# Kernel optimization log

Measured on AMD Instinct MI355X. Metric: run time of the kernel, lower is better.

## Reference

```python
import jax, jax.numpy as jnp
import numpy as np

B, L, D, K = 64, 1024, 128, 256
SQRT_2D = float(np.sqrt(2 * D))


def _biamlp(x1, x2, Wi, bi, Wq, bq):
    # proj to 2*D, norm-weighted fusion, avg-pool(2)*2 (== pairwise sum), L2-normalize over dim 1
    f1 = x1 @ Wi + bi          # [B, L, 2D]
    f2 = x2 @ Wq + bq          # [B, L, 2D]
    n1 = jnp.linalg.norm(f1)   # global L2 norm (scalar), as torch.norm(., p=2)
    n2 = jnp.linalg.norm(f2)
    e = (n1 / (n1 + n2)) * f1 + (n2 / (n1 + n2)) * f2
    b, l, c = e.shape
    z = e.reshape(b, l, c // 2, 2).mean(-1) * 2.0   # AvgPool1d(2,2) * 2 -> [B, L, D]
    denom = jnp.maximum(jnp.linalg.norm(z, axis=1, keepdims=True), 1e-12)  # F.normalize dim=1
    return z / denom


def _branch(feats, G_src, W_aff, W_c, W_lin, W_h):
    # feats: [B, L, D]; G_src: [B, L, 2D] (tensor fed to the affine projection)
    # a_j = affine(G_src^T): [B, 2D, L] @ [L, L]
    a_j = jnp.einsum('blc,lm->bcm', G_src, W_aff)            # [B, 2D, L]
    att = jnp.einsum('bld,bcl->bdc', feats, a_j) / SQRT_2D    # [B, D, 2D]
    C = jnp.tanh(att)
    H = jax.nn.relu(C @ W_c + jnp.einsum('bld,lk->bdk', feats, W_lin))  # [B, D, K]
    out = jnp.swapaxes(H @ W_h, 1, 2) + feats                 # [B, L, D]
    return out


def setup_inputs() -> dict:
    key = jax.random.key(0)
    ks = jax.random.split(key, 22)
    s = 0.02
    inp = {
        'f1_norm': jax.random.normal(ks[0], (B, L, D), jnp.float32),
        'f2_norm': jax.random.normal(ks[1], (B, L, D), jnp.float32),
        'f3_norm': jax.random.normal(ks[2], (B, L, D), jnp.float32),
        # BiAMLP params (feat_size = 128)
        'Wi': jax.random.normal(ks[3], (D, 2 * D), jnp.float32) * s,
        'bi': jax.random.normal(ks[4], (2 * D,), jnp.float32) * s,
        'Wq': jax.random.normal(ks[5], (D, 2 * D), jnp.float32) * s,
        'bq': jax.random.normal(ks[6], (2 * D,), jnp.float32) * s,
        # affine_{a,v,l}: Linear(l, l, bias=False), stored [in, out]
        'Wa_aff': jax.random.normal(ks[7], (L, L), jnp.float32) * s,
        'Wv_aff': jax.random.normal(ks[8], (L, L), jnp.float32) * s,
        'Wl_aff': jax.random.normal(ks[9], (L, L), jnp.float32) * s,
        # W_{a,v,t}: Linear(l, k)
        'W_a': jax.random.normal(ks[10], (L, K), jnp.float32) * s,
        'W_v': jax.random.normal(ks[11], (L, K), jnp.float32) * s,
        'W_t': jax.random.normal(ks[12], (L, K), jnp.float32) * s,
        # W_c{a,v,t}: Linear(2d, k)
        'W_ca': jax.random.normal(ks[13], (2 * D, K), jnp.float32) * s,
        'W_cv': jax.random.normal(ks[14], (2 * D, K), jnp.float32) * s,
        'W_ct': jax.random.normal(ks[15], (2 * D, K), jnp.float32) * s,
        # W_h{a,v,t}: Linear(k, l)
        'W_ha': jax.random.normal(ks[16], (K, L), jnp.float32) * s,
        'W_hv': jax.random.normal(ks[17], (K, L), jnp.float32) * s,
        'W_ht': jax.random.normal(ks[18], (K, L), jnp.float32) * s,
    }
    return inp


def reference(f1_norm, f2_norm, f3_norm, Wi, bi, Wq, bq, Wa_aff, Wv_aff, Wl_aff,
              W_a, W_v, W_t, W_ca, W_cv, W_ct, W_ha, W_hv, W_ht):
    txt, aud, vis = f1_norm, f2_norm, f3_norm
    # G2 = mode(txt, vis) and G3 = mode(aud, vis) are computed but unused in the
    # original (dead code); only G = G1 affects the output.
    G = _biamlp(txt, aud, Wi, bi, Wq, bq)        # [B, L, D]
    G_ag = jnp.concatenate([aud, G], axis=2)     # [B, L, 2D]
    G_lg = jnp.concatenate([txt, G], axis=2)     # [B, L, 2D]
    # NOTE: original bug preserved -- the visual branch projects G_ag (not G_vg).
    aud_out = _branch(aud, G_ag, Wa_aff, W_ca, W_a, W_ha)
    vis_out = _branch(vis, G_ag, Wv_aff, W_cv, W_v, W_hv)
    txt_out = _branch(txt, G_lg, Wl_aff, W_ct, W_t, W_ht)
    return (txt_out, aud_out, vis_out)
```

## Files before the change

### kernel.cpp

```cpp
#include <hip/hip_runtime.h>
#include <math.h>

typedef __attribute__((ext_vector_type(8))) short bf16x8;
typedef __attribute__((ext_vector_type(4))) float f32x4;

static constexpr int B_ = 64, L_ = 1024, D_ = 128, K_ = 256;
static constexpr long BLD_ = (long)B_ * L_ * D_;
static constexpr long LD_  = (long)L_ * D_;

__device__ __forceinline__ unsigned short f2b(float f) {
    unsigned int u = __builtin_bit_cast(unsigned int, f);
    u = (u + 0x7fffu + ((u >> 16) & 1u)) >> 16;
    return (unsigned short)u;
}
__device__ __forceinline__ float b2f(unsigned short h) {
    unsigned int u = ((unsigned int)h) << 16;
    return __builtin_bit_cast(float, u);
}

__device__ __forceinline__ void gl16(const unsigned short* g, unsigned short* s) {
    __builtin_amdgcn_global_load_lds(
        (const __attribute__((address_space(1))) unsigned int*)g,
        (__attribute__((address_space(3))) unsigned int*)s, 16, 0, 0);
}

struct TrEnt { const float* src; unsigned short* dst; int R, C, nb, start; };
struct TrTab { TrEnt e[14]; };

__global__ __launch_bounds__(256)
void trk(TrTab tab)
{
    __shared__ unsigned short T[64][72];
    int bid = blockIdx.x;
    int ei = 0;
    #pragma unroll
    for (int i = 1; i < 14; ++i) if (bid >= tab.e[i].start) ei = i;
    TrEnt e = tab.e[ei];
    int tile = bid - e.start;
    int ntR = e.R >> 6, ntC = e.C >> 6;
    int nt = ntR * ntC;
    int bb = tile / nt, tt = tile - bb * nt;
    int ri = tt % ntR, ci = tt / ntR;
    const float* src = e.src + (long)bb * e.R * e.C + (long)(ri * 64) * e.C + ci * 64;
    unsigned short* dst = e.dst + (long)bb * e.R * e.C + (long)(ci * 64) * e.R + ri * 64;
    int t = threadIdx.x;
    {
        int r = t >> 2, cq = t & 3;
        const float* s = src + (long)r * e.C + cq * 16;
        unsigned short tmp[16];
        #pragma unroll
        for (int f = 0; f < 4; ++f) {
            float4 v = *(const float4*)(s + f * 4);
            tmp[f*4+0]=f2b(v.x); tmp[f*4+1]=f2b(v.y); tmp[f*4+2]=f2b(v.z); tmp[f*4+3]=f2b(v.w);
        }
        *(uint4*)&T[r][cq*16]   = *(uint4*)&tmp[0];
        *(uint4*)&T[r][cq*16+8] = *(uint4*)&tmp[8];
    }
    __syncthreads();
    {
        int cr = t >> 2, rq = t & 3;
        unsigned short tmp[16];
        #pragma unroll
        for (int j = 0; j < 16; ++j) tmp[j] = T[rq*16 + j][cr];
        unsigned short* dp = dst + (long)cr * e.R + rq * 16;
        *(uint4*)&dp[0] = *(uint4*)&tmp[0];
        *(uint4*)&dp[8] = *(uint4*)&tmp[8];
    }
}

__global__ __launch_bounds__(256)
void cvt3(const float* s0, const float* s1, const float* s2,
          unsigned short* d, long n)
{
    const float* s = blockIdx.y == 0 ? s0 : blockIdx.y == 1 ? s1 : s2;
    unsigned short* dd = d + (long)blockIdx.y * n;
    long i = ((long)blockIdx.x * 256 + threadIdx.x) * 4;
    long stride = (long)gridDim.x * 1024;
    for (; i < n; i += stride) {
        float4 v = *(const float4*)&s[i];
        unsigned int w0 = (unsigned int)f2b(v.x) | ((unsigned int)f2b(v.y) << 16);
        unsigned int w1 = (unsigned int)f2b(v.z) | ((unsigned int)f2b(v.w) << 16);
        uint2 w; w.x = w0; w.y = w1;
        *(uint2*)&dd[i] = w;
    }
}

struct OpDesc {
    const unsigned short* A;
    long aOff0, aOff1, aOff2, sA;
    int lda;
    const unsigned short* B0;
    long bOff0, bOff1, bOff2, sB0;
    const unsigned short* B1;
    long sB1;
    int ldb;
    void* C;
    long sC;
    int ldc;
    const float* E0; const float* E1; const float* E2;
    float* ss;
    int Kd;
};

template<int EPI, int AF32, int TM>
__device__ __forceinline__ void gbody(const OpDesc& d, int bx, int by, int zrem,
                                      unsigned short (*As)[TM][32],
                                      unsigned short (*Bs)[128][32])
{
    const int tid = threadIdx.x;
    const long m0 = (long)bx * TM;
    const int n0 = by * 128;
    const int br = zrem >> 6, bb = zrem & 63;

    long aO = (br == 0 ? d.aOff0 : br == 1 ? d.aOff1 : d.aOff2) + (long)bb * d.sA;
    const unsigned short* A_ = d.A + aO;
    const float* Af = (const float*)d.A;
    const unsigned short* Bp;
    int nB = n0;
    if (d.B1 && n0 >= 128) { Bp = d.B1 + (long)bb * d.sB1; nB = n0 - 128; }
    else { Bp = d.B0 + (br == 0 ? d.bOff0 : br == 1 ? d.bOff1 : d.bOff2) + (long)bb * d.sB0; }

    const int w = tid >> 6, l = tid & 63;
    const int wm = (TM == 128) ? (w >> 1) : 0;
    const int wn = (TM == 128) ? (w & 1) : w;
    const int NJ = (TM == 128) ? 4 : 2;
    const int WS = (TM == 128) ? 64 : 32;
    const int fr = l & 15, kg = l >> 4;

    f32x4 acc[4][4];
    #pragma unroll
    for (int i = 0; i < 4; ++i)
        #pragma unroll
        for (int j = 0; j < 4; ++j)
            acc[i][j] = (f32x4){0.f, 0.f, 0.f, 0.f};

    auto stage = [&](int buf, int k0) {
        if (AF32) {
            int row = tid >> 1, half = tid & 1;
            const float* s = Af + (long)(m0 + row) * d.lda + k0 + half * 16;
            unsigned short tmp[16];
            #pragma unroll
            for (int f = 0; f < 4; ++f) {
                float4 v = *(const float4*)(s + f * 4);
                tmp[f*4+0]=f2b(v.x); tmp[f*4+1]=f2b(v.y); tmp[f*4+2]=f2b(v.z); tmp[f*4+3]=f2b(v.w);
            }
            *(uint4*)&As[buf][row][half*16]     = *(uint4*)&tmp[0];
            *(uint4*)&As[buf][row][half*16 + 8] = *(uint4*)&tmp[8];
        } else if (TM == 128) {
            const unsigned short* ga = A_ + (m0 + 32*w + (l >> 2)) * (long)d.lda + k0 + (l & 3) * 8;
            gl16(ga,                    &As[buf][32*w][0]);
            gl16(ga + 16*(long)d.lda,   &As[buf][32*w + 16][0]);
        } else {
            const unsigned short* ga = A_ + (m0 + 16*w + (l >> 2)) * (long)d.lda + k0 + (l & 3) * 8;
            gl16(ga, &As[buf][16*w][0]);
        }
        const unsigned short* gb = Bp + (long)(nB + 32*w + (l >> 2)) * d.ldb + k0 + (l & 3) * 8;
        gl16(gb,                  &Bs[buf][32*w][0]);
        gl16(gb + 16*(long)d.ldb, &Bs[buf][32*w + 16][0]);
    };

    auto compute = [&](int cb) {
        bf16x8 af[4], bf[4];
        #pragma unroll
        for (int i = 0; i < 4; ++i) af[i] = *(const bf16x8*)&As[cb][wm*64 + i*16 + fr][kg*8];
        #pragma unroll
        for (int j = 0; j < NJ; ++j) bf[j] = *(const bf16x8*)&Bs[cb][wn*WS + j*16 + fr][kg*8];
        #pragma unroll
        for (int i = 0; i < 4; ++i)
            #pragma unroll
            for (int j = 0; j < NJ; ++j)
                acc[i][j] = __builtin_amdgcn_mfma_f32_16x16x32_bf16(af[i], bf[j], acc[i][j], 0, 0, 0);
    };

    const int nt = d.Kd >> 5;
    stage(0, 0);
    __syncthreads();
    for (int t = 0; t < nt; ++t) {
        if (t + 1 < nt) stage((t + 1) & 1, (t + 1) << 5);
        compute(t & 1);
        __syncthreads();
    }

    if (EPI == 4) {
        unsigned short* C = (unsigned short*)d.C;
        float lss = 0.f;
        #pragma unroll
        for (int i = 0; i < 4; ++i) {
            #pragma unroll
            for (int j = 0; j < 4; ++j) {
                int cg = n0 + wn*64 + j*16 + fr;
                float bias = d.E0[cg];
                #pragma unroll
                for (int r = 0; r < 4; ++r) {
                    float v = acc[i][j][r] + bias;
                    lss += v * v;
                    float vp = v + __shfl_xor(v, 1);
                    if (!(fr & 1)) {
                        long row = m0 + wm*64 + i*16 + kg*4 + r;
                        C[row * (long)d.ldc + (cg >> 1)] = f2b(vp);
                    }
                }
            }
        }
        #pragma unroll
        for (int o = 32; o; o >>= 1) lss += __shfl_xor(lss, o);
        __shared__ float red4[4];
        if (l == 0) red4[w] = lss;
        __syncthreads();
        if (tid == 0)
            d.ss[bx * 2 + by] = red4[0] + red4[1] + red4[2] + red4[3];
    } else if (TM == 64) {
        float* eb = (float*)As;
        #pragma unroll
        for (int cc = 0; cc < 4; ++cc) {
            __syncthreads();
            #pragma unroll
            for (int j = 0; j < 2; ++j)
                #pragma unroll
                for (int r = 0; r < 4; ++r)
                    eb[(kg*4 + r)*128 + wn*32 + j*16 + fr] = acc[cc][j][r];
            __syncthreads();
            unsigned short* C = (unsigned short*)d.C + (long)zrem * d.sC;
            int colx = (tid & 15) * 8;
            int lr = tid >> 4;
            long gr = m0 + cc*16 + lr;
            long gi = gr * (long)d.ldc + n0 + colx;
            unsigned short ov[8];
            if (EPI == 2) *(uint4*)ov = *(const uint4*)&C[gi];
            unsigned short pk[8];
            #pragma unroll
            for (int e = 0; e < 8; ++e) {
                float v = eb[lr*128 + colx + e];
                if (EPI == 1) v = tanhf(v * 0.0625f);
                if (EPI == 2) v = fmaxf(v + b2f(ov[e]), 0.f);
                pk[e] = f2b(v);
            }
            *(uint4*)&C[gi] = *(uint4*)&pk[0];
        }
    } else {
        float* eb = (float*)As;
        #pragma unroll
        for (int cc = 0; cc < 4; ++cc) {
            __syncthreads();
            #pragma unroll
            for (int j = 0; j < 4; ++j)
                #pragma unroll
                for (int r = 0; r < 4; ++r)
                    eb[(wm*16 + kg*4 + r)*128 + wn*64 + j*16 + fr] = acc[cc][j][r];
            __syncthreads();
            if (EPI == 3) {
                long off = (br == 2) ? 0L : (long)(br + 1) * BLD_;
                float* Co = (float*)d.C + off + (long)bb * LD_;
                const float* Ep = (br == 0 ? d.E0 : br == 1 ? d.E1 : d.E2) + (long)bb * LD_;
                int colx = (tid & 31) * 4;
                #pragma unroll
                for (int p = 0; p < 4; ++p) {
                    int lr = (tid >> 5) + 8 * p;
                    long gr = m0 + (lr < 16 ? cc*16 + lr : 48 + cc*16 + lr);
                    long gi = gr * (long)d.ldc + n0 + colx;
                    float4 v = *(float4*)&eb[lr*128 + colx];
                    float4 e4 = *(const float4*)&Ep[gi];
                    v.x += e4.x; v.y += e4.y; v.z += e4.z; v.w += e4.w;
                    *(float4*)&Co[gi] = v;
                }
            } else {
                unsigned short* C = (unsigned short*)d.C + (long)zrem * d.sC;
                int colx = (tid & 15) * 8;
                #pragma unroll
                for (int p = 0; p < 2; ++p) {
                    int lr = (tid >> 4) + 16 * p;
                    long gr = m0 + (lr < 16 ? cc*16 + lr : 48 + cc*16 + lr);
                    long gi = gr * (long)d.ldc + n0 + colx;
                    unsigned short ov[8];
                    if (EPI == 2) *(uint4*)ov = *(const uint4*)&C[gi];
                    unsigned short pk[8];
                    #pragma unroll
                    for (int e = 0; e < 8; ++e) {
                        float v = eb[lr*128 + colx + e];
                        if (EPI == 1) v = tanhf(v * 0.0625f);
                        if (EPI == 2) v = fmaxf(v + b2f(ov[e]), 0.f);
                        pk[e] = f2b(v);
                    }
                    *(uint4*)&C[gi] = *(uint4*)&pk[0];
                }
            }
        }
    }
}

template<int EPI0, int EPI1, int AF32, int SWZ, int TM>
__global__ __launch_bounds__(256)
void mg(OpDesc d0, OpDesc d1, int zsplit)
{
    __shared__ __align__(16) unsigned short As[2][TM][32];
    __shared__ __align__(16) unsigned short Bs[2][128][32];
    int bx, by, bz;
    if (SWZ) {
        int nwg = gridDim.x * gridDim.y * gridDim.z;
        int c = blockIdx.x + gridDim.x * (blockIdx.y + gridDim.y * blockIdx.z);
        int lid = (c & 7) * (nwg >> 3) + (c >> 3);
        bx = lid % gridDim.x; lid /= gridDim.x;
        by = lid % gridDim.y; bz = lid / gridDim.y;
    } else {
        bx = blockIdx.x; by = blockIdx.y; bz = blockIdx.z;
    }
    if (bz < zsplit) gbody<EPI0, AF32, TM>(d0, bx, by, bz, As, Bs);
    else             gbody<EPI1, AF32, TM>(d1, bx, by, bz - zsplit, As, Bs);
}

__global__ __launch_bounds__(256)
void k2z(unsigned short* __restrict__ q1, const unsigned short* __restrict__ q2,
         const float* __restrict__ partial, float* __restrict__ colssP)
{
    int t = threadIdx.x;
    float a = partial[t] + partial[t + 256] + partial[t + 512] + partial[t + 768];
    float bsum = partial[1024 + t] + partial[1280 + t] + partial[1536 + t] + partial[1792 + t];
    #pragma unroll
    for (int o = 32; o; o >>= 1) { a += __shfl_xor(a, o); bsum += __shfl_xor(bsum, o); }
    __shared__ float ra[4], rb[4];
    int wv = t >> 6;
    if ((t & 63) == 0) { ra[wv] = a; rb[wv] = bsum; }
    __syncthreads();
    float n1 = sqrtf(ra[0] + ra[1] + ra[2] + ra[3]);
    float n2 = sqrtf(rb[0] + rb[1] + rb[2] + rb[3]);
    float al = n1 / (n1 + n2), be = n2 / (n1 + n2);

    int b = blockIdx.x, lc = blockIdx.y;
    int d = t & 127, ls = t >> 7;
    long base = ((long)b * L_ + (long)lc * 64) * D_;
    float acc = 0.f;
    for (int ll = ls; ll < 64; ll += 2) {
        long idx = base + (long)ll * D_ + d;
        float zv = al * b2f(q1[idx]) + be * b2f(q2[idx]);
        q1[idx] = f2b(zv);
        acc += zv * zv;
    }
    __shared__ float red[256];
    red[t] = acc;
    __syncthreads();
    if (t < 128)
        colssP[((long)b * 16 + lc) * 128 + d] = red[t] + red[t + 128];
}

__global__ __launch_bounds__(256)
void k3nT(const unsigned short* __restrict__ z, const float* __restrict__ colssP,
          unsigned short* __restrict__ GT)
{
    __shared__ unsigned short T[128][136];
    int b = blockIdx.x, lt = blockIdx.y;
    int t = threadIdx.x;
    {
        int r = t >> 1, half = t & 1;
        const unsigned short* src = z + ((long)b * L_ + lt * 128 + r) * D_ + half * 64;
        #pragma unroll
        for (int q = 0; q < 8; ++q)
            *(uint4*)&T[r][half*64 + q*8] = *(const uint4*)(src + q*8);
    }
    __syncthreads();
    {
        int d = t >> 1, lh = t & 1;
        float s = 0.f;
        #pragma unroll
        for (int lc = 0; lc < 16; ++lc)
            s += colssP[((long)b * 16 + lc) * 128 + d];
        float inv = 1.f / fmaxf(sqrtf(s), 1e-12f);
        unsigned short tmp[64];
        #pragma unroll
        for (int j = 0; j < 64; ++j) tmp[j] = f2b(b2f(T[lh*64 + j][d]) * inv);
        unsigned short* dp = GT + ((long)b * D_ + d) * L_ + lt * 128 + lh * 64;
        #pragma unroll
        for (int q = 0; q < 8; ++q) *(uint4*)&dp[q*8] = *(uint4*)&tmp[q*8];
    }
}

extern "C" void kernel_launch(void* const* d_in, const int* in_sizes, int n_in,
                              void* d_out, int out_size, void* d_ws, size_t ws_size,
                              hipStream_t stream)
{
    const float* txt = (const float*)d_in[0];
    const float* aud = (const float*)d_in[1];
    const float* vis = (const float*)d_in[2];
    const float* Wi  = (const float*)d_in[3];
    const float* bi  = (const float*)d_in[4];
    const float* Wq  = (const float*)d_in[5];
    const float* bq  = (const float*)d_in[6];
    const float* Waff[3] = { (const float*)d_in[7], (const float*)d_in[8], (const float*)d_in[9] };
    const float* Wlin[3] = { (const float*)d_in[10], (const float*)d_in[11], (const float*)d_in[12] };
    const float* Wc[3]   = { (const float*)d_in[13], (const float*)d_in[14], (const float*)d_in[15] };
    const float* Wh[3]   = { (const float*)d_in[16], (const float*)d_in[17], (const float*)d_in[18] };

    unsigned short* w16 = (unsigned short*)d_ws;
    unsigned short* featT = w16;
    unsigned short* q1b   = featT + 3 * BLD_;
    unsigned short* q2b   = q1b + BLD_;
    unsigned short* WAb   = q2b + BLD_;
    unsigned short* WLTb  = WAb + 3145728;
    unsigned short* WCTb  = WLTb + 786432;
    unsigned short* WHTb  = WCTb + 196608;
    unsigned short* WiTb  = WHTb + 786432;
    unsigned short* WqTb  = WiTb + 32768;
    float* partial = (float*)(WqTb + 32768);
    float* colssP  = partial + 2048;
    unsigned short* Cm3 = q1b;
    unsigned short* Hb3 = q1b + 6291456;
    unsigned short* S2all = (unsigned short*)d_out;
    unsigned short* GT    = S2all + 3 * BLD_;

    TrTab tab;
    auto setE = [&](int i, const float* s, unsigned short* dst, int R, int C, int nb, int start) {
        tab.e[i].src = s; tab.e[i].dst = dst; tab.e[i].R = R; tab.e[i].C = C;
        tab.e[i].nb = nb; tab.e[i].start = start;
    };
    int st = 0;
    setE(0, aud, featT + 0,        1024, 128, 64, st); st += 2048;
    setE(1, vis, featT + BLD_,     1024, 128, 64, st); st += 2048;
    setE(2, txt, featT + 2 * BLD_, 1024, 128, 64, st); st += 2048;
    setE(3, Wi, WiTb, 128, 256, 1, st); st += 8;
    setE(4, Wq, WqTb, 128, 256, 1, st); st += 8;
    for (int i = 0; i < 3; ++i) { setE(5 + i, Wlin[i], WLTb + (long)i * 262144, 1024, 256, 1, st); st += 64; }
    for (int i = 0; i < 3; ++i) { setE(8 + i, Wc[i],   WCTb + (long)i * 65536,  256, 256, 1, st); st += 16; }
    for (int i = 0; i < 3; ++i) { setE(11 + i, Wh[i],  WHTb + (long)i * 262144, 256, 1024, 1, st); st += 64; }
    trk<<<st, 256, 0, stream>>>(tab);
    cvt3<<<dim3(1024, 3), 256, 0, stream>>>(Waff[0], Waff[1], Waff[2], WAb, 1048576);

    OpDesc dTxt = {}, dAud = {};
    dTxt.A = (const unsigned short*)txt; dTxt.lda = 128;
    dTxt.B0 = WiTb; dTxt.ldb = 128;
    dTxt.C = q1b; dTxt.ldc = 128;
    dTxt.E0 = bi; dTxt.ss = partial; dTxt.Kd = 128;
    dAud = dTxt;
    dAud.A = (const unsigned short*)aud; dAud.B0 = WqTb; dAud.C = q2b;
    dAud.E0 = bq; dAud.ss = partial + 1024;
    mg<4, 4, 1, 0, 128><<<dim3(512, 2, 2), 256, 0, stream>>>(dTxt, dAud, 1);

    k2z<<<dim3(64, 16), 256, 0, stream>>>(q1b, q2b, partial, colssP);
    k3nT<<<dim3(64, 8), 256, 0, stream>>>(q1b, colssP, GT);

    OpDesc dS2 = {};
    dS2.A = featT; dS2.aOff0 = 0; dS2.aOff1 = BLD_; dS2.aOff2 = 2 * BLD_;
    dS2.sA = LD_; dS2.lda = 1024;
    dS2.B0 = WAb; dS2.bOff0 = 0; dS2.bOff1 = 1048576; dS2.bOff2 = 2097152;
    dS2.sB0 = 0; dS2.ldb = 1024;
    dS2.C = S2all; dS2.sC = LD_; dS2.ldc = 1024; dS2.Kd = 1024;
    mg<0, 0, 0, 1, 128><<<dim3(1, 8, 192), 256, 0, stream>>>(dS2, dS2, 192);

    OpDesc dAtt = {};
    dAtt.A = S2all; dAtt.aOff0 = 0; dAtt.aOff1 = 64 * LD_; dAtt.aOff2 = 128 * LD_;
    dAtt.sA = LD_; dAtt.lda = 1024;
    dAtt.B0 = featT; dAtt.bOff0 = 0; dAtt.bOff1 = 0; dAtt.bOff2 = 2 * BLD_;
    dAtt.sB0 = LD_;
    dAtt.B1 = GT; dAtt.sB1 = LD_; dAtt.ldb = 1024;
    dAtt.C = Cm3; dAtt.sC = 32768; dAtt.ldc = 256; dAtt.Kd = 1024;
    OpDesc dU = {};
    dU.A = featT; dU.aOff0 = 0; dU.aOff1 = BLD_; dU.aOff2 = 2 * BLD_;
    dU.sA = LD_; dU.lda = 1024;
    dU.B0 = WLTb; dU.bOff0 = 0; dU.bOff1 = 262144; dU.bOff2 = 524288;
    dU.sB0 = 0; dU.ldb = 1024;
    dU.C = Hb3; dU.sC = 32768; dU.ldc = 256; dU.Kd = 1024;
    mg<1, 0, 0, 1, 64><<<dim3(2, 2, 384), 256, 0, stream>>>(dAtt, dU, 192);

    OpDesc dT = {};
    dT.A = Cm3; dT.aOff0 = 0; dT.aOff1 = 2097152; dT.aOff2 = 4194304;
    dT.sA = 32768; dT.lda = 256;
    dT.B0 = WCTb; dT.bOff0 = 0; dT.bOff1 = 65536; dT.bOff2 = 131072;
    dT.sB0 = 0; dT.ldb = 256;
    dT.C = Hb3; dT.sC = 32768; dT.ldc = 256; dT.Kd = 256;
    mg<2, 2, 0, 1, 64><<<dim3(2, 2, 192), 256, 0, stream>>>(dT, dT, 192);

    OpDesc dOut = {};
    dOut.A = WHTb; dOut.aOff0 = 0; dOut.aOff1 = 262144; dOut.aOff2 = 524288;
    dOut.sA = 0; dOut.lda = 256;
    dOut.B0 = Hb3; dOut.bOff0 = 0; dOut.bOff1 = 2097152; dOut.bOff2 = 4194304;
    dOut.sB0 = 32768; dOut.ldb = 256;
    dOut.C = d_out; dOut.ldc = 128;
    dOut.E0 = aud; dOut.E1 = vis; dOut.E2 = txt; dOut.Kd = 256;
    mg<3, 3, 0, 1, 128><<<dim3(8, 1, 192), 256, 0, stream>>>(dOut, dOut, 192);
}
```

Baseline: 294.7 us.

## Swizzle LDS tiles, stage EPI4 output through LDS, fold weight convert into transpose kernel

The GEMM kernel now XOR-swizzles the column chunk index in both the global-to-LDS loads and the fragment reads, to reduce LDS bank conflicts. The EPI==4 projection epilogue writes biased accumulators to LDS and then emits packed 16-byte rows of pairwise sums, replacing the scattered 2-byte stores that used shuffles. The separate cvt3 launch for the affine weights is removed and those weights go through the transpose kernel as non-transposed entries, saving one launch. The LDS staging adds extra barriers in the epilogue, and the swizzle must agree exactly between the load and read paths.

After: 296.7 us. No clear change (+0.7%).

```diff
diff --git a/kernel.cpp b/kernel.cpp
--- a/kernel.cpp
+++ b/kernel.cpp
@@ -24,8 +24,8 @@
         (__attribute__((address_space(3))) unsigned int*)s, 16, 0, 0);
 }
 
-struct TrEnt { const float* src; unsigned short* dst; int R, C, nb, start; };
-struct TrTab { TrEnt e[14]; };
+struct TrEnt { const float* src; unsigned short* dst; int R, C, tr, start; };
+struct TrTab { TrEnt e[17]; };
 
 __global__ __launch_bounds__(256)
 void trk(TrTab tab)
@@ -34,7 +34,7 @@
     int bid = blockIdx.x;
     int ei = 0;
     #pragma unroll
-    for (int i = 1; i < 14; ++i) if (bid >= tab.e[i].start) ei = i;
+    for (int i = 1; i < 17; ++i) if (bid >= tab.e[i].start) ei = i;
     TrEnt e = tab.e[ei];
     int tile = bid - e.start;
     int ntR = e.R >> 6, ntC = e.C >> 6;
@@ -42,8 +42,23 @@
     int bb = tile / nt, tt = tile - bb * nt;
     int ri = tt % ntR, ci = tt / ntR;
     const float* src = e.src + (long)bb * e.R * e.C + (long)(ri * 64) * e.C + ci * 64;
+    int t = threadIdx.x;
+    if (!e.tr) {
+        unsigned short* dstd = e.dst + (long)bb * e.R * e.C + (long)(ri * 64) * e.C + ci * 64;
+        int r = t >> 2, cq = t & 3;
+        const float* s = src + (long)r * e.C + cq * 16;
+        unsigned short tmp[16];
+        #pragma unroll
+        for (int f = 0; f < 4; ++f) {
+            float4 v = *(const float4*)(s + f * 4);
+            tmp[f*4+0]=f2b(v.x); tmp[f*4+1]=f2b(v.y); tmp[f*4+2]=f2b(v.z); tmp[f*4+3]=f2b(v.w);
+        }
+        unsigned short* dp = dstd + (long)r * e.C + cq * 16;
+        *(uint4*)&dp[0] = *(uint4*)&tmp[0];
+        *(uint4*)&dp[8] = *(uint4*)&tmp[8];
+        return;
+    }
     unsigned short* dst = e.dst + (long)bb * e.R * e.C + (long)(ci * 64) * e.R + ri * 64;
-    int t = threadIdx.x;
     {
         int r = t >> 2, cq = t & 3;
         const float* s = src + (long)r * e.C + cq * 16;
@@ -65,23 +80,6 @@
         unsigned short* dp = dst + (long)cr * e.R + rq * 16;
         *(uint4*)&dp[0] = *(uint4*)&tmp[0];
         *(uint4*)&dp[8] = *(uint4*)&tmp[8];
-    }
-}
-
-__global__ __launch_bounds__(256)
-void cvt3(const float* s0, const float* s1, const float* s2,
-          unsigned short* d, long n)
-{
-    const float* s = blockIdx.y == 0 ? s0 : blockIdx.y == 1 ? s1 : s2;
-    unsigned short* dd = d + (long)blockIdx.y * n;
-    long i = ((long)blockIdx.x * 256 + threadIdx.x) * 4;
-    long stride = (long)gridDim.x * 1024;
-    for (; i < n; i += stride) {
-        float4 v = *(const float4*)&s[i];
-        unsigned int w0 = (unsigned int)f2b(v.x) | ((unsigned int)f2b(v.y) << 16);
-        unsigned int w1 = (unsigned int)f2b(v.z) | ((unsigned int)f2b(v.w) << 16);
-        uint2 w; w.x = w0; w.y = w1;
-        *(uint2*)&dd[i] = w;
     }
 }
 
@@ -134,6 +132,9 @@
         for (int j = 0; j < 4; ++j)
             acc[i][j] = (f32x4){0.f, 0.f, 0.f, 0.f};
 
+    const int sc8 = ((l & 3) ^ ((l >> 3) & 3)) * 8;
+    const int rc  = (kg ^ ((fr >> 1) & 3)) * 8;
+
     auto stage = [&](int buf, int k0) {
         if (AF32) {
             int row = tid >> 1, half = tid & 1;
@@ -144,17 +145,18 @@
                 float4 v = *(const float4*)(s + f * 4);
                 tmp[f*4+0]=f2b(v.x); tmp[f*4+1]=f2b(v.y); tmp[f*4+2]=f2b(v.z); tmp[f*4+3]=f2b(v.w);
             }
-            *(uint4*)&As[buf][row][half*16]     = *(uint4*)&tmp[0];
-            *(uint4*)&As[buf][row][half*16 + 8] = *(uint4*)&tmp[8];
+            int sw = (row >> 1) & 3;
+            *(uint4*)&As[buf][row][((2*half    ) ^ sw) * 8] = *(uint4*)&tmp[0];
+            *(uint4*)&As[buf][row][((2*half + 1) ^ sw) * 8] = *(uint4*)&tmp[8];
         } else if (TM == 128) {
-            const unsigned short* ga = A_ + (m0 + 32*w + (l >> 2)) * (long)d.lda + k0 + (l & 3) * 8;
+            const unsigned short* ga = A_ + (m0 + 32*w + (l >> 2)) * (long)d.lda + k0 + sc8;
             gl16(ga,                    &As[buf][32*w][0]);
             gl16(ga + 16*(long)d.lda,   &As[buf][32*w + 16][0]);
         } else {
-            const unsigned short* ga = A_ + (m0 + 16*w + (l >> 2)) * (long)d.lda + k0 + (l & 3) * 8;
+            const unsigned short* ga = A_ + (m0 + 16*w + (l >> 2)) * (long)d.lda + k0 + sc8;
             gl16(ga, &As[buf][16*w][0]);
         }
-        const unsigned short* gb = Bp + (long)(nB + 32*w + (l >> 2)) * d.ldb + k0 + (l & 3) * 8;
+        const unsigned short* gb = Bp + (long)(nB + 32*w + (l >> 2)) * d.ldb + k0 + sc8;
         gl16(gb,                  &Bs[buf][32*w][0]);
         gl16(gb + 16*(long)d.ldb, &Bs[buf][32*w + 16][0]);
     };
@@ -162,9 +164,9 @@
     auto compute = [&](int cb) {
         bf16x8 af[4], bf[4];
         #pragma unroll
-        for (int i = 0; i < 4; ++i) af[i] = *(const bf16x8*)&As[cb][wm*64 + i*16 + fr][kg*8];
-        #pragma unroll
-        for (int j = 0; j < NJ; ++j) bf[j] = *(const bf16x8*)&Bs[cb][wn*WS + j*16 + fr][kg*8];
+        for (int i = 0; i < 4; ++i) af[i] = *(const bf16x8*)&As[cb][wm*64 + i*16 + fr][rc];
+        #pragma unroll
+        for (int j = 0; j < NJ; ++j) bf[j] = *(const bf16x8*)&Bs[cb][wn*WS + j*16 + fr][rc];
         #pragma unroll
         for (int i = 0; i < 4; ++i)
             #pragma unroll
@@ -185,7 +187,7 @@
         unsigned short* C = (unsigned short*)d.C;
         float lss = 0.f;
         #pragma unroll
-        for (int i = 0; i < 4; ++i) {
+        for (int i = 0; i < 4; ++i)
             #pragma unroll
             for (int j = 0; j < 4; ++j) {
                 int cg = n0 + wn*64 + j*16 + fr;
@@ -194,19 +196,36 @@
                 for (int r = 0; r < 4; ++r) {
                     float v = acc[i][j][r] + bias;
                     lss += v * v;
-                    float vp = v + __shfl_xor(v, 1);
-                    if (!(fr & 1)) {
-                        long row = m0 + wm*64 + i*16 + kg*4 + r;
-                        C[row * (long)d.ldc + (cg >> 1)] = f2b(vp);
-                    }
                 }
             }
-        }
         #pragma unroll
         for (int o = 32; o; o >>= 1) lss += __shfl_xor(lss, o);
         __shared__ float red4[4];
         if (l == 0) red4[w] = lss;
-        __syncthreads();
+        float* eb = (float*)As;
+        #pragma unroll
+        for (int cc = 0; cc < 4; ++cc) {
+            __syncthreads();
+            #pragma unroll
+            for (int j = 0; j < 4; ++j) {
+                int cg = n0 + wn*64 + j*16 + fr;
+                float bias = d.E0[cg];
+                #pragma unroll
+                for (int r = 0; r < 4; ++r)
+                    eb[(wm*16 + kg*4 + r)*128 + wn*64 + j*16 + fr] = acc[cc][j][r] + bias;
+            }
+            __syncthreads();
+            int lr = tid >> 3, pc = tid & 7;
+            long gr = m0 + (lr < 16 ? cc*16 + lr : 48 + cc*16 + lr);
+            unsigned short pk[8];
+            #pragma unroll
+            for (int e = 0; e < 8; ++e) {
+                float v0 = eb[lr*128 + pc*16 + 2*e];
+                float v1 = eb[lr*128 + pc*16 + 2*e + 1];
+                pk[e] = f2b(v0 + v1);
+            }
+            *(uint4*)&C[gr * (long)d.ldc + (n0 >> 1) + pc*8] = *(uint4*)&pk[0];
+        }
         if (tid == 0)
             d.ss[bx * 2 + by] = red4[0] + red4[1] + red4[2] + red4[3];
     } else if (TM == 64) {
@@ -407,21 +426,21 @@
     unsigned short* GT    = S2all + 3 * BLD_;
 
     TrTab tab;
-    auto setE = [&](int i, const float* s, unsigned short* dst, int R, int C, int nb, int start) {
+    auto setE = [&](int i, const float* s, unsigned short* dst, int R, int C, int tr, int start) {
         tab.e[i].src = s; tab.e[i].dst = dst; tab.e[i].R = R; tab.e[i].C = C;
-        tab.e[i].nb = nb; tab.e[i].start = start;
+        tab.e[i].tr = tr; tab.e[i].start = start;
     };
     int st = 0;
-    setE(0, aud, featT + 0,        1024, 128, 64, st); st += 2048;
-    setE(1, vis, featT + BLD_,     1024, 128, 64, st); st += 2048;
-    setE(2, txt, featT + 2 * BLD_, 1024, 128, 64, st); st += 2048;
+    setE(0, aud, featT + 0,        1024, 128, 1, st); st += 2048;
+    setE(1, vis, featT + BLD_,     1024, 128, 1, st); st += 2048;
+    setE(2, txt, featT + 2 * BLD_, 1024, 128, 1, st); st += 2048;
     setE(3, Wi, WiTb, 128, 256, 1, st); st += 8;
     setE(4, Wq, WqTb, 128, 256, 1, st); st += 8;
     for (int i = 0; i < 3; ++i) { setE(5 + i, Wlin[i], WLTb + (long)i * 262144, 1024, 256, 1, st); st += 64; }
     for (int i = 0; i < 3; ++i) { setE(8 + i, Wc[i],   WCTb + (long)i * 65536,  256, 256, 1, st); st += 16; }
     for (int i = 0; i < 3; ++i) { setE(11 + i, Wh[i],  WHTb + (long)i * 262144, 256, 1024, 1, st); st += 64; }
+    for (int i = 0; i < 3; ++i) { setE(14 + i, Waff[i], WAb + (long)i * 1048576, 1024, 1024, 0, st); st += 256; }
     trk<<<st, 256, 0, stream>>>(tab);
-    cvt3<<<dim3(1024, 3), 256, 0, stream>>>(Waff[0], Waff[1], Waff[2], WAb, 1048576);
 
     OpDesc dTxt = {}, dAud = {};
     dTxt.A = (const unsigned short*)txt; dTxt.lda = 128;
```
